# Performance work log

Hardware: AMD Instinct MI355X
Metric: run time of the kernel (lower is better)

Reference implementation:

```python
import jax, jax.numpy as jnp
import numpy as np

THRESHOLD = 1.0
SLOPE = 25.0  # snntorch surrogate.fast_sigmoid default

@jax.custom_vjp
def spike_fn(x):
    # heaviside forward, fast_sigmoid surrogate backward
    return (x > 0).astype(x.dtype)

def _spike_fwd(x):
    return spike_fn(x), x

def _spike_bwd(x, g):
    return (g / (SLOPE * jnp.abs(x) + 1.0) ** 2,)

spike_fn.defvjp(_spike_fwd, _spike_bwd)


def setup_inputs() -> dict:
    key = jax.random.key(0)
    ks = jax.random.split(key, 8)
    B, D_IN, H0, H1 = 16384, 512, 1024, 512
    def linear_params(kw, kb, fan_in, fan_out):
        bound = 1.0 / np.sqrt(fan_in)
        w = jax.random.uniform(kw, (fan_out, fan_in), jnp.float32, -bound, bound)
        b = jax.random.uniform(kb, (fan_out,), jnp.float32, -bound, bound)
        return w, b
    w1, b1 = linear_params(ks[0], ks[1], D_IN, H0)
    w2, b2 = linear_params(ks[2], ks[3], H0, H1)
    w3, b3 = linear_params(ks[4], ks[5], H1, 1)
    data = jax.random.normal(ks[6], (B, D_IN), jnp.float32)
    return {"data": data, "w1": w1, "b1": b1, "w2": w2, "b2": b2,
            "w3": w3, "b3": b3, "time_steps": 8}


def reference(data, w1, b1, w2, b2, w3, b3, time_steps):
    # Effective betas: snntorch clamps beta to [0,1]. lif1 beta = units0 (=1024) -> 1.0 (source bug, replicated).
    beta1 = jnp.float32(1.0)
    beta2 = jnp.float32(0.95)
    # data is constant across time, so fc1 output is step-invariant
    cur1 = data @ w1.T + b1                      # [B, H0]
    B, H0 = cur1.shape
    H1 = w2.shape[0]
    mem1_0 = jnp.zeros((B, H0), cur1.dtype)
    mem2_0 = jnp.zeros((B, H1), cur1.dtype)

    def step(carry, _):
        mem1, mem2 = carry
        # snntorch Leaky (reset_mechanism='subtract'): reset detected on OLD mem, detached
        reset1 = jax.lax.stop_gradient((mem1 > THRESHOLD).astype(mem1.dtype))
        mem1 = beta1 * mem1 + cur1 - reset1 * THRESHOLD
        spk1 = spike_fn(mem1 - THRESHOLD)
        cur2 = spk1 @ w2.T + b2                  # [B, H1]
        reset2 = jax.lax.stop_gradient((mem2 > THRESHOLD).astype(mem2.dtype))
        mem2 = beta2 * mem2 + cur2 - reset2 * THRESHOLD
        spk2 = spike_fn(mem2 - THRESHOLD)
        cur3 = spk2 @ w3.T + b3                  # [B, 1]
        return (mem1, mem2), cur3

    _, cur3_seq = jax.lax.scan(step, (mem1_0, mem2_0), None, length=time_steps)
    return jnp.mean(cur3_seq, axis=0)            # [B, 1]
```

## Files before the change

kernel.cpp:

```cpp
#include <hip/hip_runtime.h>
#include <hip/hip_bf16.h>
#include <cstdint>
#include <cstddef>


#define NB 16384
#define DIN 512
#define NH0 1024
#define NH1 512

typedef float f32x4 __attribute__((ext_vector_type(4)));
typedef short bf16x8 __attribute__((ext_vector_type(8)));

#define WS_PAT   0u
#define WS_W2H   19922944u
#define WS_W2M   20971520u
#define WS_W2L   22020096u

__device__ inline uint16_t f2bf(float f) {
    __hip_bfloat16 h = __float2bfloat16(f);
    return *reinterpret_cast<uint16_t*>(&h);
}
__device__ inline float bf2f(uint16_t u) {
    __hip_bfloat16 h = *reinterpret_cast<__hip_bfloat16*>(&u);
    return __bfloat162float(h);
}

__global__ void init_out_kernel(float* __restrict__ out,
                                const float* __restrict__ b3, int n) {
    int i = blockIdx.x * blockDim.x + threadIdx.x;
    if (i < n) out[i] = b3[0];
}

__global__ __launch_bounds__(256) void split3_kernel(
    const float* __restrict__ src, uint16_t* __restrict__ h,
    uint16_t* __restrict__ m, uint16_t* __restrict__ l, int n)
{
    int i = (blockIdx.x * 256 + threadIdx.x) * 4;
    if (i >= n) return;
    float4 f = *(const float4*)(src + i);
    float fv[4] = {f.x, f.y, f.z, f.w};
    uint32_t hw[2], mw[2], lw[2];
    #pragma unroll
    for (int g = 0; g < 2; ++g) {
        uint16_t hh[2], mm[2], ll[2];
        #pragma unroll
        for (int e = 0; e < 2; ++e) {
            float a = fv[2 * g + e];
            uint16_t h0 = f2bf(a);
            float d = __fsub_rn(a, bf2f(h0));
            uint16_t m0 = f2bf(d);
            float e2 = __fsub_rn(d, bf2f(m0));
            uint16_t l0 = f2bf(e2);
            hh[e] = h0; mm[e] = m0; ll[e] = l0;
        }
        hw[g] = (uint32_t)hh[0] | ((uint32_t)hh[1] << 16);
        mw[g] = (uint32_t)mm[0] | ((uint32_t)mm[1] << 16);
        lw[g] = (uint32_t)ll[0] | ((uint32_t)ll[1] << 16);
    }
    *(uint2*)(h + i) = make_uint2(hw[0], hw[1]);
    *(uint2*)(m + i) = make_uint2(mw[0], mw[1]);
    *(uint2*)(l + i) = make_uint2(lw[0], lw[1]);
}

__global__ __launch_bounds__(256, 2) void gemm1_spike_kernel(
    const float* __restrict__ data, const float* __restrict__ w1,
    const float* __restrict__ b1, uint8_t* __restrict__ pat)
{
    __shared__ float As[128][68];
    __shared__ float Bs[128][68];
    const int tid = threadIdx.x;
    const int tx = tid & 15, ty = tid >> 4;
    const int i0 = blockIdx.x * 128, n0 = blockIdx.y * 128;

    float acc[8][8] = {};

    for (int kb = 0; kb < DIN; kb += 64) {
        #pragma unroll
        for (int rep = 0; rep < 8; ++rep) {
            int idx = tid + rep * 256;
            int row = idx >> 4, c4 = (idx & 15) * 4;
            *(float4*)(&As[row][c4]) =
                *(const float4*)(data + (size_t)(i0 + row) * DIN + kb + c4);
            *(float4*)(&Bs[row][c4]) =
                *(const float4*)(w1 + (size_t)(n0 + row) * DIN + kb + c4);
        }
        __syncthreads();
        #pragma unroll 2
        for (int k4 = 0; k4 < 16; ++k4) {
            float4 a4[8], b4[8];
            #pragma unroll
            for (int ii = 0; ii < 8; ++ii)
                a4[ii] = *(const float4*)(&As[ty + ii * 16][k4 * 4]);
            #pragma unroll
            for (int nn = 0; nn < 8; ++nn)
                b4[nn] = *(const float4*)(&Bs[tx + nn * 16][k4 * 4]);
            #pragma unroll
            for (int ii = 0; ii < 8; ++ii) {
                #pragma unroll
                for (int nn = 0; nn < 8; ++nn) {
                    acc[ii][nn] = fmaf(a4[ii].x, b4[nn].x, acc[ii][nn]);
                    acc[ii][nn] = fmaf(a4[ii].y, b4[nn].y, acc[ii][nn]);
                    acc[ii][nn] = fmaf(a4[ii].z, b4[nn].z, acc[ii][nn]);
                    acc[ii][nn] = fmaf(a4[ii].w, b4[nn].w, acc[ii][nn]);
                }
            }
        }
        __syncthreads();
    }

    #pragma unroll
    for (int ii = 0; ii < 8; ++ii) {
        const int i = i0 + ty + ii * 16;
        #pragma unroll
        for (int nn = 0; nn < 8; ++nn) {
            const int n = n0 + tx + nn * 16;
            float x = __fadd_rn(acc[ii][nn], b1[n]);
            float mem = 0.0f;
            unsigned p = 0;
            #pragma unroll
            for (int t = 0; t < 8; ++t) {
                bool reset = mem > 1.0f;
                float tmp = __fadd_rn(mem, x);
                mem = reset ? __fsub_rn(tmp, 1.0f) : tmp;
                p |= (mem > 1.0f ? 1u : 0u) << t;
            }
            pat[(size_t)(n >> 6) * (NB * 64) + (size_t)i * 64 + (n & 63)] = (uint8_t)p;
        }
    }
}

__global__ __launch_bounds__(256, 2) void gemm2_mfma_kernel(
    const uint8_t* __restrict__ pat,
    const uint16_t* __restrict__ w2h, const uint16_t* __restrict__ w2m,
    const uint16_t* __restrict__ w2l,
    const float* __restrict__ b2, const float* __restrict__ w3,
    float* __restrict__ out)
{
    __shared__ __align__(16) uint16_t Bhi[64][72];
    __shared__ __align__(16) uint16_t Bmd[64][72];
    __shared__ __align__(16) uint16_t Blo[64][72];
    __shared__ __align__(16) uint8_t  Ap[64][80];

    const int tid  = threadIdx.x;
    const int lane = tid & 63;
    const int wv   = tid >> 6;
    const int lr   = lane & 15;
    const int lg   = lane >> 4;
    const int i0   = blockIdx.x * 64, n0 = blockIdx.y * 64;

    f32x4 acc[8][4];
    #pragma unroll
    for (int t = 0; t < 8; ++t)
        #pragma unroll
        for (int nf = 0; nf < 4; ++nf)
            acc[t][nf] = (f32x4)(0.0f);

    const int srow = tid >> 2;
    const int scol = (tid & 3) * 16;

    for (int kb = 0; kb < NH0; kb += 64) {
        __syncthreads();
        const uint16_t* s1 = w2h + (size_t)(n0 + srow) * NH0 + kb + scol;
        const uint16_t* s2 = w2m + (size_t)(n0 + srow) * NH0 + kb + scol;
        const uint16_t* s3 = w2l + (size_t)(n0 + srow) * NH0 + kb + scol;
        *(uint4*)(&Bhi[srow][scol])     = *(const uint4*)(s1);
        *(uint4*)(&Bhi[srow][scol + 8]) = *(const uint4*)(s1 + 8);
        *(uint4*)(&Bmd[srow][scol])     = *(const uint4*)(s2);
        *(uint4*)(&Bmd[srow][scol + 8]) = *(const uint4*)(s2 + 8);
        *(uint4*)(&Blo[srow][scol])     = *(const uint4*)(s3);
        *(uint4*)(&Blo[srow][scol + 8]) = *(const uint4*)(s3 + 8);
        {
            const uint8_t* psrc = pat + (size_t)(kb >> 6) * (NB * 64) + (size_t)i0 * 64;
            uint4 pv = *(const uint4*)(psrc + tid * 16);
            *(uint4*)(&Ap[srow][scol]) = pv;
        }
        __syncthreads();

        #pragma unroll
        for (int s = 0; s < 2; ++s) {
            const int k0 = s * 32;
            bf16x8 bh[4], bm[4], bl[4];
            #pragma unroll
            for (int nf = 0; nf < 4; ++nf) {
                const int col = nf * 16 + lr;
                bh[nf] = *(const bf16x8*)(&Bhi[col][k0 + lg * 8]);
                bm[nf] = *(const bf16x8*)(&Bmd[col][k0 + lg * 8]);
                bl[nf] = *(const bf16x8*)(&Blo[col][k0 + lg * 8]);
            }
            const uint2 p8 = *(const uint2*)(&Ap[wv * 16 + lr][k0 + lg * 8]);
            #pragma unroll
            for (int t = 0; t < 8; ++t) {
                uint32_t y0 = (p8.x >> t) & 0x01010101u;
                uint32_t y1 = (p8.y >> t) & 0x01010101u;
                uint32_t s0 = __builtin_amdgcn_perm(0u, y0, 0x01010000u) | 0x02000200u;
                uint32_t s1x = __builtin_amdgcn_perm(0u, y0, 0x03030202u) | 0x02000200u;
                uint32_t s2x = __builtin_amdgcn_perm(0u, y1, 0x01010000u) | 0x02000200u;
                uint32_t s3x = __builtin_amdgcn_perm(0u, y1, 0x03030202u) | 0x02000200u;
                union { uint4 u; bf16x8 v; } af;
                af.u = make_uint4(__builtin_amdgcn_perm(0u, 0x3F008000u, s0),
                                  __builtin_amdgcn_perm(0u, 0x3F008000u, s1x),
                                  __builtin_amdgcn_perm(0u, 0x3F008000u, s2x),
                                  __builtin_amdgcn_perm(0u, 0x3F008000u, s3x));
                #pragma unroll
                for (int nf = 0; nf < 4; ++nf) {
                    acc[t][nf] = __builtin_amdgcn_mfma_f32_16x16x32_bf16(
                        af.v, bh[nf], acc[t][nf], 0, 0, 0);
                    acc[t][nf] = __builtin_amdgcn_mfma_f32_16x16x32_bf16(
                        af.v, bm[nf], acc[t][nf], 0, 0, 0);
                    acc[t][nf] = __builtin_amdgcn_mfma_f32_16x16x32_bf16(
                        af.v, bl[nf], acc[t][nf], 0, 0, 0);
                }
            }
        }
    }

    float rowsum[4] = {0.0f, 0.0f, 0.0f, 0.0f};
    #pragma unroll
    for (int nf = 0; nf < 4; ++nf) {
        const int n = n0 + nf * 16 + lr;
        const float b2n = b2[n];
        const float w3n = w3[n];
        #pragma unroll
        for (int r = 0; r < 4; ++r) {
            float mem = 0.0f;
            int pc = 0;
            #pragma unroll
            for (int t = 0; t < 8; ++t) {
                bool reset = mem > 1.0f;
                float x   = __fadd_rn(acc[t][nf][r], b2n);
                float tmp = __fadd_rn(__fmul_rn(0.95f, mem), x);
                mem = reset ? __fsub_rn(tmp, 1.0f) : tmp;
                pc += (mem > 1.0f) ? 1 : 0;
            }
            rowsum[r] = fmaf(w3n, (float)pc, rowsum[r]);
        }
    }
    #pragma unroll
    for (int r = 0; r < 4; ++r) {
        float s = rowsum[r];
        s += __shfl_xor(s, 1);
        s += __shfl_xor(s, 2);
        s += __shfl_xor(s, 4);
        s += __shfl_xor(s, 8);
        if (lr == 0)
            atomicAdd(&out[i0 + wv * 16 + lg * 4 + r], 0.125f * s);
    }
}

extern "C" void kernel_launch(void* const* d_in, const int* in_sizes, int n_in,
                              void* d_out, int out_size, void* d_ws, size_t ws_size,
                              hipStream_t stream) {
    const float* data = (const float*)d_in[0];
    const float* w1   = (const float*)d_in[1];
    const float* b1   = (const float*)d_in[2];
    const float* w2   = (const float*)d_in[3];
    const float* b2   = (const float*)d_in[4];
    const float* w3   = (const float*)d_in[5];
    const float* b3   = (const float*)d_in[6];
    float* out = (float*)d_out;

    char* ws = (char*)d_ws;
    uint8_t*  pat = (uint8_t*)(ws + WS_PAT);
    uint16_t* w2h = (uint16_t*)(ws + WS_W2H);
    uint16_t* w2m = (uint16_t*)(ws + WS_W2M);
    uint16_t* w2l = (uint16_t*)(ws + WS_W2L);

    init_out_kernel<<<(NB + 255) / 256, 256, 0, stream>>>(out, b3, NB);
    split3_kernel<<<(NH1 * NH0 / 4 + 255) / 256, 256, 0, stream>>>(w2, w2h, w2m, w2l, NH1 * NH0);
    gemm1_spike_kernel<<<dim3(NB / 128, NH0 / 128), 256, 0, stream>>>(data, w1, b1, pat);
    gemm2_mfma_kernel<<<dim3(NB / 64, NH1 / 64), 256, 0, stream>>>(pat, w2h, w2m, w2l, b2, w3, out);
}
```

Before: 617.7 us.

## Double-buffer gemm2 tiles via register prefetch and retile gemm1 to 512 threads

The MFMA GEMM kernel now prefetches the next k-block of the split-bf16 W2 tiles and the spike patterns into registers while computing on the current LDS buffer. It then writes them into a second LDS buffer, cutting one barrier per iteration and hiding global load latency. Separately, the fp32 GEMM1 kernel moves to 512 threads per block with 8x4 outputs per thread instead of 8x8, with launch bounds of 4 blocks. That launch bound may force a tight register cap and spilling, and LDS use still limits real occupancy.

```diff
diff --git a/kernel.cpp b/kernel.cpp
--- a/kernel.cpp
+++ b/kernel.cpp
@@ -63,22 +63,23 @@
     *(uint2*)(l + i) = make_uint2(lw[0], lw[1]);
 }
 
-__global__ __launch_bounds__(256, 2) void gemm1_spike_kernel(
+__global__ __launch_bounds__(512, 4) void gemm1_spike_kernel(
     const float* __restrict__ data, const float* __restrict__ w1,
     const float* __restrict__ b1, uint8_t* __restrict__ pat)
 {
     __shared__ float As[128][68];
     __shared__ float Bs[128][68];
     const int tid = threadIdx.x;
-    const int tx = tid & 15, ty = tid >> 4;
+    const int tx = tid & 31;
+    const int ty = tid >> 5;
     const int i0 = blockIdx.x * 128, n0 = blockIdx.y * 128;
 
-    float acc[8][8] = {};
+    float acc[8][4] = {};
 
     for (int kb = 0; kb < DIN; kb += 64) {
         #pragma unroll
-        for (int rep = 0; rep < 8; ++rep) {
-            int idx = tid + rep * 256;
+        for (int rep = 0; rep < 4; ++rep) {
+            int idx = tid + rep * 512;
             int row = idx >> 4, c4 = (idx & 15) * 4;
             *(float4*)(&As[row][c4]) =
                 *(const float4*)(data + (size_t)(i0 + row) * DIN + kb + c4);
@@ -88,17 +89,17 @@
         __syncthreads();
         #pragma unroll 2
         for (int k4 = 0; k4 < 16; ++k4) {
-            float4 a4[8], b4[8];
+            float4 a4[8], b4[4];
             #pragma unroll
             for (int ii = 0; ii < 8; ++ii)
                 a4[ii] = *(const float4*)(&As[ty + ii * 16][k4 * 4]);
             #pragma unroll
-            for (int nn = 0; nn < 8; ++nn)
-                b4[nn] = *(const float4*)(&Bs[tx + nn * 16][k4 * 4]);
+            for (int nn = 0; nn < 4; ++nn)
+                b4[nn] = *(const float4*)(&Bs[tx + nn * 32][k4 * 4]);
             #pragma unroll
             for (int ii = 0; ii < 8; ++ii) {
                 #pragma unroll
-                for (int nn = 0; nn < 8; ++nn) {
+                for (int nn = 0; nn < 4; ++nn) {
                     acc[ii][nn] = fmaf(a4[ii].x, b4[nn].x, acc[ii][nn]);
                     acc[ii][nn] = fmaf(a4[ii].y, b4[nn].y, acc[ii][nn]);
                     acc[ii][nn] = fmaf(a4[ii].z, b4[nn].z, acc[ii][nn]);
@@ -113,8 +114,8 @@
     for (int ii = 0; ii < 8; ++ii) {
         const int i = i0 + ty + ii * 16;
         #pragma unroll
-        for (int nn = 0; nn < 8; ++nn) {
-            const int n = n0 + tx + nn * 16;
+        for (int nn = 0; nn < 4; ++nn) {
+            const int n = n0 + tx + nn * 32;
             float x = __fadd_rn(acc[ii][nn], b1[n]);
             float mem = 0.0f;
             unsigned p = 0;
@@ -137,10 +138,10 @@
     const float* __restrict__ b2, const float* __restrict__ w3,
     float* __restrict__ out)
 {
-    __shared__ __align__(16) uint16_t Bhi[64][72];
-    __shared__ __align__(16) uint16_t Bmd[64][72];
-    __shared__ __align__(16) uint16_t Blo[64][72];
-    __shared__ __align__(16) uint8_t  Ap[64][80];
+    __shared__ __align__(16) uint16_t Bhi[2][64][72];
+    __shared__ __align__(16) uint16_t Bmd[2][64][72];
+    __shared__ __align__(16) uint16_t Blo[2][64][72];
+    __shared__ __align__(16) uint8_t  Ap[2][64][80];
 
     const int tid  = threadIdx.x;
     const int lane = tid & 63;
@@ -158,24 +159,41 @@
 
     const int srow = tid >> 2;
     const int scol = (tid & 3) * 16;
-
-    for (int kb = 0; kb < NH0; kb += 64) {
+    const size_t wbase = (size_t)(n0 + srow) * NH0 + scol;
+    const size_t pbase = (size_t)i0 * 64 + (size_t)tid * 16;
+
+    uint4 rh0, rh1, rm0, rm1, rl0, rl1, rp;
+
+    {
+        const uint16_t* s1 = w2h + wbase;
+        const uint16_t* s2 = w2m + wbase;
+        const uint16_t* s3 = w2l + wbase;
+        rh0 = *(const uint4*)(s1); rh1 = *(const uint4*)(s1 + 8);
+        rm0 = *(const uint4*)(s2); rm1 = *(const uint4*)(s2 + 8);
+        rl0 = *(const uint4*)(s3); rl1 = *(const uint4*)(s3 + 8);
+        rp  = *(const uint4*)(pat + pbase);
+        *(uint4*)(&Bhi[0][srow][scol])     = rh0;
+        *(uint4*)(&Bhi[0][srow][scol + 8]) = rh1;
+        *(uint4*)(&Bmd[0][srow][scol])     = rm0;
+        *(uint4*)(&Bmd[0][srow][scol + 8]) = rm1;
+        *(uint4*)(&Blo[0][srow][scol])     = rl0;
+        *(uint4*)(&Blo[0][srow][scol + 8]) = rl1;
+        *(uint4*)(&Ap[0][srow][scol])      = rp;
+    }
+
+    int cur = 0;
+    for (int kbi = 0; kbi < 16; ++kbi) {
         __syncthreads();
-        const uint16_t* s1 = w2h + (size_t)(n0 + srow) * NH0 + kb + scol;
-        const uint16_t* s2 = w2m + (size_t)(n0 + srow) * NH0 + kb + scol;
-        const uint16_t* s3 = w2l + (size_t)(n0 + srow) * NH0 + kb + scol;
-        *(uint4*)(&Bhi[srow][scol])     = *(const uint4*)(s1);
-        *(uint4*)(&Bhi[srow][scol + 8]) = *(const uint4*)(s1 + 8);
-        *(uint4*)(&Bmd[srow][scol])     = *(const uint4*)(s2);
-        *(uint4*)(&Bmd[srow][scol + 8]) = *(const uint4*)(s2 + 8);
-        *(uint4*)(&Blo[srow][scol])     = *(const uint4*)(s3);
-        *(uint4*)(&Blo[srow][scol + 8]) = *(const uint4*)(s3 + 8);
-        {
-            const uint8_t* psrc = pat + (size_t)(kb >> 6) * (NB * 64) + (size_t)i0 * 64;
-            uint4 pv = *(const uint4*)(psrc + tid * 16);
-            *(uint4*)(&Ap[srow][scol]) = pv;
-        }
-        __syncthreads();
+        if (kbi < 15) {
+            const int kb = (kbi + 1) * 64;
+            const uint16_t* s1 = w2h + wbase + kb;
+            const uint16_t* s2 = w2m + wbase + kb;
+            const uint16_t* s3 = w2l + wbase + kb;
+            rh0 = *(const uint4*)(s1); rh1 = *(const uint4*)(s1 + 8);
+            rm0 = *(const uint4*)(s2); rm1 = *(const uint4*)(s2 + 8);
+            rl0 = *(const uint4*)(s3); rl1 = *(const uint4*)(s3 + 8);
+            rp  = *(const uint4*)(pat + (size_t)(kbi + 1) * (NB * 64) + pbase);
+        }
 
         #pragma unroll
         for (int s = 0; s < 2; ++s) {
@@ -184,11 +202,11 @@
             #pragma unroll
             for (int nf = 0; nf < 4; ++nf) {
                 const int col = nf * 16 + lr;
-                bh[nf] = *(const bf16x8*)(&Bhi[col][k0 + lg * 8]);
-                bm[nf] = *(const bf16x8*)(&Bmd[col][k0 + lg * 8]);
-                bl[nf] = *(const bf16x8*)(&Blo[col][k0 + lg * 8]);
-            }
-            const uint2 p8 = *(const uint2*)(&Ap[wv * 16 + lr][k0 + lg * 8]);
+                bh[nf] = *(const bf16x8*)(&Bhi[cur][col][k0 + lg * 8]);
+                bm[nf] = *(const bf16x8*)(&Bmd[cur][col][k0 + lg * 8]);
+                bl[nf] = *(const bf16x8*)(&Blo[cur][col][k0 + lg * 8]);
+            }
+            const uint2 p8 = *(const uint2*)(&Ap[cur][wv * 16 + lr][k0 + lg * 8]);
             #pragma unroll
             for (int t = 0; t < 8; ++t) {
                 uint32_t y0 = (p8.x >> t) & 0x01010101u;
@@ -213,6 +231,18 @@
                 }
             }
         }
+
+        if (kbi < 15) {
+            const int nb = cur ^ 1;
+            *(uint4*)(&Bhi[nb][srow][scol])     = rh0;
+            *(uint4*)(&Bhi[nb][srow][scol + 8]) = rh1;
+            *(uint4*)(&Bmd[nb][srow][scol])     = rm0;
+            *(uint4*)(&Bmd[nb][srow][scol + 8]) = rm1;
+            *(uint4*)(&Blo[nb][srow][scol])     = rl0;
+            *(uint4*)(&Blo[nb][srow][scol + 8]) = rl1;
+            *(uint4*)(&Ap[nb][srow][scol])      = rp;
+        }
+        cur ^= 1;
     }
 
     float rowsum[4] = {0.0f, 0.0f, 0.0f, 0.0f};
@@ -268,6 +298,6 @@
 
     init_out_kernel<<<(NB + 255) / 256, 256, 0, stream>>>(out, b3, NB);
     split3_kernel<<<(NH1 * NH0 / 4 + 255) / 256, 256, 0, stream>>>(w2, w2h, w2m, w2l, NH1 * NH0);
-    gemm1_spike_kernel<<<dim3(NB / 128, NH0 / 128), 256, 0, stream>>>(data, w1, b1, pat);
+    gemm1_spike_kernel<<<dim3(NB / 128, NH0 / 128), 512, 0, stream>>>(data, w1, b1, pat);
     gemm2_mfma_kernel<<<dim3(NB / 64, NH1 / 64), 256, 0, stream>>>(pat, w2h, w2m, w2l, b2, w3, out);
 }
```

Measured after the change: 563.1 us. 8.8% less time.
